# Kernel optimization log

Measured on AMD Instinct MI355X. Metric: run time of the kernel, lower is better.

## Reference

```python
import jax, jax.numpy as jnp
import numpy as np

N_HEAD = 16


def setup_inputs() -> dict:
    key = jax.random.key(0)
    k1, k2, k3 = jax.random.split(key, 3)
    B, T, C = 2, 2048, 1024
    x = jax.random.normal(k1, (B, T, C), dtype=jnp.float32)
    w_attn = jax.random.normal(k2, (C, 3 * C), dtype=jnp.float32) * 0.02
    w_proj = jax.random.normal(k3, (C, C), dtype=jnp.float32) * 0.02
    return {"x": x, "w_attn": w_attn, "w_proj": w_proj}


def reference(x, w_attn, w_proj):
    B, T, C = x.shape
    H = N_HEAD
    D = C // H
    qkv = x @ w_attn  # [B, T, 3C]
    q, k, v = jnp.split(qkv, 3, axis=2)
    q = q.reshape(B, T, H, D)
    k = k.reshape(B, T, H, D)
    v = v.reshape(B, T, H, D)
    scale = 1.0 / jnp.sqrt(jnp.asarray(D, dtype=x.dtype))
    # Full T x T score matrix, matching the 'standard_attention' path.
    att = jnp.einsum('bthd,bshd->bhts', q, k) * scale  # [B, H, T, T]
    causal = jnp.tril(jnp.ones((T, T), dtype=bool))
    att = jnp.where(causal[None, None, :, :], att, jnp.asarray(-jnp.inf, dtype=att.dtype))
    att = jax.nn.softmax(att, axis=-1)
    # dropout_p is False (== 0.0) in the original module, so no dropout applied.
    y = jnp.einsum('bhts,bshd->bthd', att, v)  # [B, T, H, D]
    y = y.reshape(B, T, C)
    return y @ w_proj
```

## Files before the change

### kernel.cpp

```cpp
#include <hip/hip_runtime.h>
#include <math.h>

#define BB 2
#define TT 2048
#define HH 16
#define DD 64
#define CC 1024
#define C3 3072

typedef __attribute__((ext_vector_type(8))) short bf16x8;
typedef __attribute__((ext_vector_type(4))) short bf16x4;
typedef __attribute__((ext_vector_type(4))) float f32x4;
typedef __attribute__((ext_vector_type(2))) unsigned int u32x2;

__device__ __forceinline__ unsigned short f2bf(float f) {
  union { float f; unsigned u; } v; v.f = f;
  unsigned r = v.u + 0x7fffu + ((v.u >> 16) & 1u);
  return (unsigned short)(r >> 16);
}
__device__ __forceinline__ unsigned short f2bf_up(float f) {
  union { float f; unsigned u; } v; v.f = f;
  return (unsigned short)((v.u + 0x8000u) >> 16);
}

__device__ __forceinline__ void async_cp16(const void* g, void* l) {
  __builtin_amdgcn_global_load_lds(
      (const __attribute__((address_space(1))) void*)g,
      (__attribute__((address_space(3))) void*)l, 16, 0, 0);
}

__global__ __launch_bounds__(256)
void prep(const float* __restrict__ x, const float* __restrict__ w_attn,
          const float* __restrict__ w_proj, unsigned short* __restrict__ xb,
          unsigned short* __restrict__ wat, unsigned short* __restrict__ wpt) {
  __shared__ __align__(16) float Ts[64][68];
  const int bx = blockIdx.x, tid = threadIdx.x;
  if (bx < 1024) {
    int i = bx * 256 + tid;
#pragma unroll
    for (int it = 0; it < 4; ++it, i += 262144) {
      const float4 v = ((const float4*)x)[i];
      bf16x4 o = {(short)f2bf(v.x), (short)f2bf(v.y),
                  (short)f2bf(v.z), (short)f2bf(v.w)};
      ((bf16x4*)xb)[i] = o;
    }
    return;
  }
  const float* W;
  unsigned short* WT;
  int Nd, bound, n0, k0;
  float s;
  if (bx < 1792) {
    const int bid = bx - 1024;
    W = w_attn; WT = wat; Nd = 3072; bound = 1024; s = 0.18033688f;
    n0 = (bid % 48) * 64; k0 = (bid / 48) * 64;
  } else {
    const int bid = bx - 1792;
    W = w_proj; WT = wpt; Nd = 1024; bound = 0; s = 1.0f;
    n0 = (bid % 16) * 64; k0 = (bid / 16) * 64;
  }
  const int rl = tid >> 4, c4 = tid & 15;
#pragma unroll
  for (int it = 0; it < 4; ++it) {
    const int r = it * 16 + rl;
    *(float4*)&Ts[r][c4 * 4] =
        *(const float4*)(W + (size_t)(k0 + r) * Nd + n0 + c4 * 4);
  }
  __syncthreads();
#pragma unroll
  for (int it = 0; it < 4; ++it) {
    const int n = it * 16 + rl;
    const float sc = (n0 + n < bound) ? s : 1.0f;
    bf16x4 o = {(short)f2bf(Ts[c4 * 4 + 0][n] * sc),
                (short)f2bf(Ts[c4 * 4 + 1][n] * sc),
                (short)f2bf(Ts[c4 * 4 + 2][n] * sc),
                (short)f2bf(Ts[c4 * 4 + 3][n] * sc)};
    *(bf16x4*)(WT + (size_t)(n0 + n) * CC + k0 + c4 * 4) = o;
  }
}

template <int MODE, int BM>
__global__ __launch_bounds__(256)
void gemm_bf16(const unsigned short* __restrict__ A,
               const unsigned short* __restrict__ BT,
               void* __restrict__ Cout, unsigned short* __restrict__ Vout,
               int M, int N, int K) {
  constexpr int MT = BM / 32;
  constexpr int ABYTES = BM * 64;
  __shared__ __align__(16) unsigned short As[2 * BM * 32];
  __shared__ __align__(16) unsigned short Bs[2 * 128 * 32];

  const int tid = threadIdx.x;
  const int w = tid >> 6, lane = tid & 63;
  const int l15 = lane & 15, quad = lane >> 4;
  const int wm = w >> 1, wn = w & 1;

  const int row0 = blockIdx.y * BM, col0 = blockIdx.x * 128;

  const int c0 = tid, c1 = tid + 256;
  const int ar0 = c0 >> 2, ak0 = ((c0 & 3) ^ ((c0 >> 3) & 3)) * 8;
  const int ar1 = c1 >> 2, ak1 = ((c1 & 3) ^ ((c1 >> 3) & 3)) * 8;
  const unsigned short* gA0 = A + (size_t)(row0 + ar0) * K + ak0;
  const unsigned short* gA1 = A + (size_t)(row0 + ar1) * K + ak1;
  const unsigned short* gB0 = BT + (size_t)(col0 + ar0) * K + ak0;
  const unsigned short* gB1 = BT + (size_t)(col0 + ar1) * K + ak1;
  const int lds0 = w * 1024, lds1 = 4096 + w * 1024;

  const int fro = l15 * 64 + 16 * (quad ^ ((l15 >> 1) & 3));

  f32x4 acc[MT][4];
#pragma unroll
  for (int i = 0; i < MT; ++i)
#pragma unroll
    for (int j = 0; j < 4; ++j) acc[i][j] = (f32x4){0.f, 0.f, 0.f, 0.f};

  const int nt = K / 32;
  async_cp16(gA0, (char*)As + lds0);
  if (BM == 128) async_cp16(gA1, (char*)As + lds1);
  async_cp16(gB0, (char*)Bs + lds0);
  async_cp16(gB1, (char*)Bs + lds1);

  for (int i = 0; i < nt; ++i) {
    const int cur = i & 1;
    __syncthreads();

    if (i + 1 < nt) {
      const int k1 = (i + 1) * 32;
      const int alt = cur ^ 1;
      async_cp16(gA0 + k1, (char*)As + alt * ABYTES + lds0);
      if (BM == 128) async_cp16(gA1 + k1, (char*)As + alt * ABYTES + lds1);
      async_cp16(gB0 + k1, (char*)Bs + alt * 8192 + lds0);
      async_cp16(gB1 + k1, (char*)Bs + alt * 8192 + lds1);
    }

    const char* fA = (const char*)As + cur * ABYTES + wm * (BM * 32) + fro;
    const char* fB = (const char*)Bs + cur * 8192 + wn * 4096 + fro;

    bf16x8 af[MT], bf[4];
#pragma unroll
    for (int mt = 0; mt < MT; ++mt) af[mt] = *(const bf16x8*)(fA + mt * 1024);
#pragma unroll
    for (int nt2 = 0; nt2 < 4; ++nt2) bf[nt2] = *(const bf16x8*)(fB + nt2 * 1024);
#pragma unroll
    for (int mt = 0; mt < MT; ++mt)
#pragma unroll
      for (int nt2 = 0; nt2 < 4; ++nt2)
        acc[mt][nt2] = __builtin_amdgcn_mfma_f32_16x16x32_bf16(
            af[mt], bf[nt2], acc[mt][nt2], 0, 0, 0);
  }

  if (MODE == 2 && col0 >= 2048) {
#pragma unroll
    for (int mt = 0; mt < MT; ++mt) {
      const int rbase = row0 + wm * (BM / 2) + mt * 16 + quad * 4;
      const int bq = rbase >> 11, t0 = rbase & 2047;
#pragma unroll
      for (int nt2 = 0; nt2 < 4; ++nt2) {
        const int col = col0 + wn * 64 + nt2 * 16 + l15;
        bf16x4 o = {(short)f2bf(acc[mt][nt2][0]), (short)f2bf(acc[mt][nt2][1]),
                    (short)f2bf(acc[mt][nt2][2]), (short)f2bf(acc[mt][nt2][3])};
        *(bf16x4*)(Vout + ((size_t)((bq << 10) + col - 2048) << 11) + t0) = o;
      }
    }
  } else if (MODE >= 1) {
    unsigned short* Cb = (unsigned short*)Cout;
#pragma unroll
    for (int mt = 0; mt < MT; ++mt) {
      const int rbase = row0 + wm * (BM / 2) + mt * 16 + quad * 4;
#pragma unroll
      for (int r = 0; r < 4; ++r) {
        unsigned short* cr = Cb + (size_t)(rbase + r) * N + col0 + wn * 64 + l15;
#pragma unroll
        for (int nt2 = 0; nt2 < 4; ++nt2) cr[nt2 * 16] = f2bf(acc[mt][nt2][r]);
      }
    }
  } else {
    float* Cf = (float*)Cout;
#pragma unroll
    for (int mt = 0; mt < MT; ++mt) {
      const int rbase = row0 + wm * (BM / 2) + mt * 16 + quad * 4;
#pragma unroll
      for (int r = 0; r < 4; ++r) {
        float* cr = Cf + (size_t)(rbase + r) * N + col0 + wn * 64 + l15;
#pragma unroll
        for (int nt2 = 0; nt2 < 4; ++nt2) cr[nt2 * 16] = acc[mt][nt2][r];
      }
    }
  }
}

__global__ __launch_bounds__(256)
void attn_mfma(const unsigned short* __restrict__ qkvb,
               const unsigned short* __restrict__ vt,
               unsigned short* __restrict__ y) {
  const int n = blockIdx.x;
  const int bh = (n & 7) + 8 * ((n >> 3) & 3);
  const int qpair = n >> 5;
  const int b = bh >> 4, h = bh & 15;
  const int tid = threadIdx.x;
  const int w = tid >> 6;
  const int lane = tid & 63;
  const int l15 = lane & 15, quad = lane >> 4;

  __shared__ __align__(16) char Kb[2 * 8192];
  __shared__ __align__(16) char Vb[2 * 8192];
  __shared__ __align__(16) unsigned short Ps[4 * 16 * 72];
  unsigned short* psw = Ps + w * 16 * 72;

  const int lr = lane >> 3;
  const int lc = lane & 7;
  const int srcoff = ((lc ^ lr) << 4);
  const char* ksrc = (const char*)qkvb + ((size_t)(b * TT) * C3 + 1024 + h * 64) * 2;
  const char* vsrc = (const char*)vt + ((size_t)(b * HH + h) * DD * TT) * 2;

  const int fro = l15 * 128 + ((quad ^ (l15 & 7)) << 4);

  bf16x8 onesf;
#pragma unroll
  for (int jj = 0; jj < 8; ++jj) onesf[jj] = (short)0x3F80;

  for (int phase = 0; phase < 2; ++phase) {
    const int qt = phase == 0 ? 31 - qpair : qpair;

    if (phase) __syncthreads();

    const unsigned short* qrow =
        qkvb + (size_t)(b * TT + qt * 64 + w * 16 + l15) * C3 + h * DD;
    bf16x8 qf0 = *(const bf16x8*)(qrow + quad * 8);
    bf16x8 qf1 = *(const bf16x8*)(qrow + 32 + quad * 8);

    f32x4 O[4];
#pragma unroll
    for (int dt = 0; dt < 4; ++dt) O[dt] = (f32x4){0.f, 0.f, 0.f, 0.f};
    f32x4 lacc = (f32x4){0.f, 0.f, 0.f, 0.f};

#pragma unroll
    for (int i = 0; i < 2; ++i) {
      async_cp16(ksrc + (size_t)(w * 16 + i * 8 + lr) * (C3 * 2) + srcoff,
                 Kb + w * 2048 + i * 1024);
      async_cp16(vsrc + (size_t)(w * 16 + i * 8 + lr) * (TT * 2) + srcoff,
                 Vb + w * 2048 + i * 1024);
    }

    for (int j = 0; j <= qt; ++j) {
      const int cur = j & 1;
      __syncthreads();

      if (j < qt) {
        const int key1 = (j + 1) * 64;
        char* kd = Kb + (cur ^ 1) * 8192 + w * 2048;
        char* vd = Vb + (cur ^ 1) * 8192 + w * 2048;
#pragma unroll
        for (int i = 0; i < 2; ++i) {
          async_cp16(
              ksrc + (size_t)(key1 + w * 16 + i * 8 + lr) * (C3 * 2) + srcoff,
              kd + i * 1024);
          async_cp16(
              vsrc + (size_t)(w * 16 + i * 8 + lr) * (TT * 2) + key1 * 2 + srcoff,
              vd + i * 1024);
        }
      }

      const char* Kc = Kb + cur * 8192;
      const char* Vc = Vb + cur * 8192;

      f32x4 S[4];
#pragma unroll
      for (int ct = 0; ct < 4; ++ct) {
        bf16x8 k0 = *(const bf16x8*)(Kc + ct * 2048 + fro);
        bf16x8 k1 = *(const bf16x8*)(Kc + ct * 2048 + (fro ^ 64));
        f32x4 z = (f32x4){-12.f, -12.f, -12.f, -12.f};
        z = __builtin_amdgcn_mfma_f32_16x16x32_bf16(k0, qf0, z, 0, 0, 0);
        z = __builtin_amdgcn_mfma_f32_16x16x32_bf16(k1, qf1, z, 0, 0, 0);
        S[ct] = z;
      }

      if (j == qt) {
#pragma unroll
        for (int ct = 0; ct < 4; ++ct)
#pragma unroll
          for (int r = 0; r < 4; ++r)
            if (16 * ct + quad * 4 + r > w * 16 + l15) S[ct][r] = -INFINITY;
      }

#pragma unroll
      for (int ct = 0; ct < 4; ++ct) {
        const unsigned p0 = f2bf_up(exp2f(S[ct][0]));
        const unsigned p1 = f2bf_up(exp2f(S[ct][1]));
        const unsigned p2 = f2bf_up(exp2f(S[ct][2]));
        const unsigned p3 = f2bf_up(exp2f(S[ct][3]));
        u32x2 d;
        d[0] = p0 | (p1 << 16);
        d[1] = p2 | (p3 << 16);
        *(u32x2*)((char*)psw + l15 * 144 + ct * 32 + quad * 8) = d;
      }

      bf16x8 pf0 = *(const bf16x8*)((char*)psw + l15 * 144 + quad * 16);
      bf16x8 pf1 = *(const bf16x8*)((char*)psw + l15 * 144 + 64 + quad * 16);

      lacc = __builtin_amdgcn_mfma_f32_16x16x32_bf16(onesf, pf0, lacc, 0, 0, 0);
      lacc = __builtin_amdgcn_mfma_f32_16x16x32_bf16(onesf, pf1, lacc, 0, 0, 0);
#pragma unroll
      for (int dt = 0; dt < 4; ++dt) {
        bf16x8 v0 = *(const bf16x8*)(Vc + dt * 2048 + fro);
        bf16x8 v1 = *(const bf16x8*)(Vc + dt * 2048 + (fro ^ 64));
        O[dt] = __builtin_amdgcn_mfma_f32_16x16x32_bf16(v0, pf0, O[dt], 0, 0, 0);
        O[dt] = __builtin_amdgcn_mfma_f32_16x16x32_bf16(v1, pf1, O[dt], 0, 0, 0);
      }
    }

    const float inv = 1.0f / lacc[0];
    unsigned short* yr =
        y + (size_t)(b * TT + qt * 64 + w * 16 + l15) * CC + h * DD + quad * 4;
#pragma unroll
    for (int dt = 0; dt < 4; ++dt) {
      bf16x4 o = {(short)f2bf(O[dt][0] * inv), (short)f2bf(O[dt][1] * inv),
                  (short)f2bf(O[dt][2] * inv), (short)f2bf(O[dt][3] * inv)};
      *(bf16x4*)(yr + dt * 16) = o;
    }
  }
}

extern "C" void kernel_launch(void* const* d_in, const int* in_sizes, int n_in,
                              void* d_out, int out_size, void* d_ws,
                              size_t ws_size, hipStream_t stream) {
  const float* x      = (const float*)d_in[0];
  const float* w_attn = (const float*)d_in[1];
  const float* w_proj = (const float*)d_in[2];
  float* out = (float*)d_out;

  unsigned short* xb   = (unsigned short*)d_ws;
  unsigned short* wat  = xb + (size_t)4096 * 1024;
  unsigned short* wpt  = wat + (size_t)3072 * 1024;
  unsigned short* qkvb = wpt + (size_t)1024 * 1024;
  unsigned short* vt   = qkvb + (size_t)4096 * 3072;
  unsigned short* yb   = vt + (size_t)BB * HH * DD * TT;

  dim3 blk(256);

  prep<<<2048, blk, 0, stream>>>(x, w_attn, w_proj, xb, wat, wpt);

  gemm_bf16<2, 128><<<dim3(C3 / 128, (BB * TT) / 128), blk, 0, stream>>>(
      xb, wat, qkvb, vt, BB * TT, C3, CC);

  attn_mfma<<<dim3(512, 1, 1), blk, 0, stream>>>(qkvb, vt, yb);

  gemm_bf16<0, 64><<<dim3(CC / 128, (BB * TT) / 64), blk, 0, stream>>>(
      yb, wpt, out, nullptr, BB * TT, CC, CC);
}
```

Before: 192.0 us.

## Specialize QKV and output GEMMs with retuned tiles and deeper K-steps

Replaces the templated GEMM with two dedicated kernels. The QKV GEMM now uses 128x192 tiles, giving 16x32=512 blocks (previously 24x32=768), with each wave covering all 128 rows and 48 columns. The output projection GEMM uses a K-step of 64 with a wider XOR swizzle, halving the number of barrier and loop iterations. Both kernels request two blocks per CU through launch bounds, and the larger accumulator arrays may raise register pressure.

```diff
diff --git a/kernel.cpp b/kernel.cpp
--- a/kernel.cpp
+++ b/kernel.cpp
@@ -79,112 +79,185 @@
   }
 }
 
-template <int MODE, int BM>
-__global__ __launch_bounds__(256)
-void gemm_bf16(const unsigned short* __restrict__ A,
-               const unsigned short* __restrict__ BT,
-               void* __restrict__ Cout, unsigned short* __restrict__ Vout,
-               int M, int N, int K) {
-  constexpr int MT = BM / 32;
-  constexpr int ABYTES = BM * 64;
-  __shared__ __align__(16) unsigned short As[2 * BM * 32];
-  __shared__ __align__(16) unsigned short Bs[2 * 128 * 32];
+__global__ __launch_bounds__(256, 2)
+void gemm_qkv(const unsigned short* __restrict__ A,
+              const unsigned short* __restrict__ BT,
+              unsigned short* __restrict__ Cb,
+              unsigned short* __restrict__ Vout) {
+  __shared__ __align__(16) unsigned short As[2 * 128 * 32];
+  __shared__ __align__(16) unsigned short Bs[2 * 192 * 32];
+
+  const int tid = threadIdx.x;
+  const int w = tid >> 6, lane = tid & 63;
+  const int l15 = lane & 15, quad = lane >> 4;
+  const int row0 = blockIdx.y * 128, col0 = blockIdx.x * 192;
+
+  const int ca0 = tid, ca1 = tid + 256;
+  const int ra0 = ca0 >> 2, ka0 = ((ca0 & 3) ^ ((ca0 >> 3) & 3)) * 8;
+  const int ra1 = ca1 >> 2, ka1 = ((ca1 & 3) ^ ((ca1 >> 3) & 3)) * 8;
+  const unsigned short* gA0 = A + (size_t)(row0 + ra0) * CC + ka0;
+  const unsigned short* gA1 = A + (size_t)(row0 + ra1) * CC + ka1;
+  const int cb0 = tid, cb1 = tid + 256, cb2 = tid + 512;
+  const int rb0 = cb0 >> 2, kb0 = ((cb0 & 3) ^ ((cb0 >> 3) & 3)) * 8;
+  const int rb1 = cb1 >> 2, kb1 = ((cb1 & 3) ^ ((cb1 >> 3) & 3)) * 8;
+  const int rb2 = cb2 >> 2, kb2 = ((cb2 & 3) ^ ((cb2 >> 3) & 3)) * 8;
+  const unsigned short* gB0 = BT + (size_t)(col0 + rb0) * CC + kb0;
+  const unsigned short* gB1 = BT + (size_t)(col0 + rb1) * CC + kb1;
+  const unsigned short* gB2 = BT + (size_t)(col0 + rb2) * CC + kb2;
+  const int la0 = tid * 16, la1 = tid * 16 + 4096;
+  const int lb0 = tid * 16, lb1 = tid * 16 + 4096, lb2 = tid * 16 + 8192;
+
+  const int fro = l15 * 64 + 16 * (quad ^ ((l15 >> 1) & 3));
+
+  f32x4 acc[8][3];
+#pragma unroll
+  for (int i = 0; i < 8; ++i)
+#pragma unroll
+    for (int j = 0; j < 3; ++j) acc[i][j] = (f32x4){0.f, 0.f, 0.f, 0.f};
+
+  async_cp16(gA0, (char*)As + la0);
+  async_cp16(gA1, (char*)As + la1);
+  async_cp16(gB0, (char*)Bs + lb0);
+  async_cp16(gB1, (char*)Bs + lb1);
+  async_cp16(gB2, (char*)Bs + lb2);
+
+  for (int i = 0; i < 32; ++i) {
+    const int cur = i & 1;
+    __syncthreads();
+
+    if (i + 1 < 32) {
+      const int k1 = (i + 1) * 32;
+      const int ab = (cur ^ 1) * 8192, bb = (cur ^ 1) * 12288;
+      async_cp16(gA0 + k1, (char*)As + ab + la0);
+      async_cp16(gA1 + k1, (char*)As + ab + la1);
+      async_cp16(gB0 + k1, (char*)Bs + bb + lb0);
+      async_cp16(gB1 + k1, (char*)Bs + bb + lb1);
+      async_cp16(gB2 + k1, (char*)Bs + bb + lb2);
+    }
+
+    const char* fA = (const char*)As + cur * 8192 + fro;
+    const char* fB = (const char*)Bs + cur * 12288 + w * 3072 + fro;
+
+    bf16x8 af[8], bf[3];
+#pragma unroll
+    for (int mt = 0; mt < 8; ++mt) af[mt] = *(const bf16x8*)(fA + mt * 1024);
+#pragma unroll
+    for (int nt = 0; nt < 3; ++nt) bf[nt] = *(const bf16x8*)(fB + nt * 1024);
+#pragma unroll
+    for (int mt = 0; mt < 8; ++mt)
+#pragma unroll
+      for (int nt = 0; nt < 3; ++nt)
+        acc[mt][nt] = __builtin_amdgcn_mfma_f32_16x16x32_bf16(
+            af[mt], bf[nt], acc[mt][nt], 0, 0, 0);
+  }
+
+#pragma unroll
+  for (int mt = 0; mt < 8; ++mt) {
+    const int rbase = row0 + mt * 16 + quad * 4;
+#pragma unroll
+    for (int nt = 0; nt < 3; ++nt) {
+      const int colb = col0 + w * 48 + nt * 16;
+      if (colb >= 2048) {
+        const int bq = rbase >> 11, t0 = rbase & 2047;
+        const int d = colb + l15 - 2048;
+        bf16x4 o = {(short)f2bf(acc[mt][nt][0]), (short)f2bf(acc[mt][nt][1]),
+                    (short)f2bf(acc[mt][nt][2]), (short)f2bf(acc[mt][nt][3])};
+        *(bf16x4*)(Vout + (((size_t)(bq << 10) + d) << 11) + t0) = o;
+      } else {
+        const int col = colb + l15;
+#pragma unroll
+        for (int r = 0; r < 4; ++r)
+          Cb[(size_t)(rbase + r) * C3 + col] = f2bf(acc[mt][nt][r]);
+      }
+    }
+  }
+}
+
+__global__ __launch_bounds__(256, 2)
+void gemm_out(const unsigned short* __restrict__ A,
+              const unsigned short* __restrict__ BT,
+              float* __restrict__ Cf) {
+  __shared__ __align__(16) unsigned short As[2 * 64 * 64];
+  __shared__ __align__(16) unsigned short Bs[2 * 128 * 64];
 
   const int tid = threadIdx.x;
   const int w = tid >> 6, lane = tid & 63;
   const int l15 = lane & 15, quad = lane >> 4;
   const int wm = w >> 1, wn = w & 1;
-
-  const int row0 = blockIdx.y * BM, col0 = blockIdx.x * 128;
-
-  const int c0 = tid, c1 = tid + 256;
-  const int ar0 = c0 >> 2, ak0 = ((c0 & 3) ^ ((c0 >> 3) & 3)) * 8;
-  const int ar1 = c1 >> 2, ak1 = ((c1 & 3) ^ ((c1 >> 3) & 3)) * 8;
-  const unsigned short* gA0 = A + (size_t)(row0 + ar0) * K + ak0;
-  const unsigned short* gA1 = A + (size_t)(row0 + ar1) * K + ak1;
-  const unsigned short* gB0 = BT + (size_t)(col0 + ar0) * K + ak0;
-  const unsigned short* gB1 = BT + (size_t)(col0 + ar1) * K + ak1;
-  const int lds0 = w * 1024, lds1 = 4096 + w * 1024;
-
-  const int fro = l15 * 64 + 16 * (quad ^ ((l15 >> 1) & 3));
-
-  f32x4 acc[MT][4];
-#pragma unroll
-  for (int i = 0; i < MT; ++i)
+  const int row0 = blockIdx.y * 64, col0 = blockIdx.x * 128;
+
+  const int ca0 = tid, ca1 = tid + 256;
+  const int ra0 = ca0 >> 3, ka0 = ((ca0 & 7) ^ ((ca0 >> 3) & 7)) * 8;
+  const int ra1 = ca1 >> 3, ka1 = ((ca1 & 7) ^ ((ca1 >> 3) & 7)) * 8;
+  const unsigned short* gA0 = A + (size_t)(row0 + ra0) * CC + ka0;
+  const unsigned short* gA1 = A + (size_t)(row0 + ra1) * CC + ka1;
+  const unsigned short* gB[4];
+  int lb[4];
+#pragma unroll
+  for (int t = 0; t < 4; ++t) {
+    const int c = tid + t * 256;
+    const int rb = c >> 3, kb = ((c & 7) ^ ((c >> 3) & 7)) * 8;
+    gB[t] = BT + (size_t)(col0 + rb) * CC + kb;
+    lb[t] = c * 16;
+  }
+  const int la0 = tid * 16, la1 = tid * 16 + 4096;
+
+  const int fro = l15 * 128 + ((quad ^ (l15 & 7)) << 4);
+
+  f32x4 acc[2][4];
+#pragma unroll
+  for (int i = 0; i < 2; ++i)
 #pragma unroll
     for (int j = 0; j < 4; ++j) acc[i][j] = (f32x4){0.f, 0.f, 0.f, 0.f};
 
-  const int nt = K / 32;
-  async_cp16(gA0, (char*)As + lds0);
-  if (BM == 128) async_cp16(gA1, (char*)As + lds1);
-  async_cp16(gB0, (char*)Bs + lds0);
-  async_cp16(gB1, (char*)Bs + lds1);
-
-  for (int i = 0; i < nt; ++i) {
+  async_cp16(gA0, (char*)As + la0);
+  async_cp16(gA1, (char*)As + la1);
+#pragma unroll
+  for (int t = 0; t < 4; ++t) async_cp16(gB[t], (char*)Bs + lb[t]);
+
+  for (int i = 0; i < 16; ++i) {
     const int cur = i & 1;
     __syncthreads();
 
-    if (i + 1 < nt) {
-      const int k1 = (i + 1) * 32;
-      const int alt = cur ^ 1;
-      async_cp16(gA0 + k1, (char*)As + alt * ABYTES + lds0);
-      if (BM == 128) async_cp16(gA1 + k1, (char*)As + alt * ABYTES + lds1);
-      async_cp16(gB0 + k1, (char*)Bs + alt * 8192 + lds0);
-      async_cp16(gB1 + k1, (char*)Bs + alt * 8192 + lds1);
-    }
-
-    const char* fA = (const char*)As + cur * ABYTES + wm * (BM * 32) + fro;
-    const char* fB = (const char*)Bs + cur * 8192 + wn * 4096 + fro;
-
-    bf16x8 af[MT], bf[4];
-#pragma unroll
-    for (int mt = 0; mt < MT; ++mt) af[mt] = *(const bf16x8*)(fA + mt * 1024);
-#pragma unroll
-    for (int nt2 = 0; nt2 < 4; ++nt2) bf[nt2] = *(const bf16x8*)(fB + nt2 * 1024);
-#pragma unroll
-    for (int mt = 0; mt < MT; ++mt)
-#pragma unroll
-      for (int nt2 = 0; nt2 < 4; ++nt2)
-        acc[mt][nt2] = __builtin_amdgcn_mfma_f32_16x16x32_bf16(
-            af[mt], bf[nt2], acc[mt][nt2], 0, 0, 0);
-  }
-
-  if (MODE == 2 && col0 >= 2048) {
-#pragma unroll
-    for (int mt = 0; mt < MT; ++mt) {
-      const int rbase = row0 + wm * (BM / 2) + mt * 16 + quad * 4;
-      const int bq = rbase >> 11, t0 = rbase & 2047;
-#pragma unroll
-      for (int nt2 = 0; nt2 < 4; ++nt2) {
-        const int col = col0 + wn * 64 + nt2 * 16 + l15;
-        bf16x4 o = {(short)f2bf(acc[mt][nt2][0]), (short)f2bf(acc[mt][nt2][1]),
-                    (short)f2bf(acc[mt][nt2][2]), (short)f2bf(acc[mt][nt2][3])};
-        *(bf16x4*)(Vout + ((size_t)((bq << 10) + col - 2048) << 11) + t0) = o;
-      }
-    }
-  } else if (MODE >= 1) {
-    unsigned short* Cb = (unsigned short*)Cout;
-#pragma unroll
-    for (int mt = 0; mt < MT; ++mt) {
-      const int rbase = row0 + wm * (BM / 2) + mt * 16 + quad * 4;
-#pragma unroll
-      for (int r = 0; r < 4; ++r) {
-        unsigned short* cr = Cb + (size_t)(rbase + r) * N + col0 + wn * 64 + l15;
-#pragma unroll
-        for (int nt2 = 0; nt2 < 4; ++nt2) cr[nt2 * 16] = f2bf(acc[mt][nt2][r]);
-      }
-    }
-  } else {
-    float* Cf = (float*)Cout;
-#pragma unroll
-    for (int mt = 0; mt < MT; ++mt) {
-      const int rbase = row0 + wm * (BM / 2) + mt * 16 + quad * 4;
-#pragma unroll
-      for (int r = 0; r < 4; ++r) {
-        float* cr = Cf + (size_t)(rbase + r) * N + col0 + wn * 64 + l15;
-#pragma unroll
-        for (int nt2 = 0; nt2 < 4; ++nt2) cr[nt2 * 16] = acc[mt][nt2][r];
-      }
+    if (i + 1 < 16) {
+      const int k1 = (i + 1) * 64;
+      const int ab = (cur ^ 1) * 8192, bb = (cur ^ 1) * 16384;
+      async_cp16(gA0 + k1, (char*)As + ab + la0);
+      async_cp16(gA1 + k1, (char*)As + ab + la1);
+#pragma unroll
+      for (int t = 0; t < 4; ++t) async_cp16(gB[t] + k1, (char*)Bs + bb + lb[t]);
+    }
+
+    const char* fA = (const char*)As + cur * 8192 + wm * 4096 + fro;
+    const char* fB = (const char*)Bs + cur * 16384 + wn * 8192 + fro;
+
+#pragma unroll
+    for (int kh = 0; kh < 2; ++kh) {
+      const int xo = kh * 64;
+      bf16x8 af[2], bf[4];
+#pragma unroll
+      for (int mt = 0; mt < 2; ++mt)
+        af[mt] = *(const bf16x8*)(fA + mt * 2048 + ((fro + xo) & 127) - (fro & 127));
+#pragma unroll
+      for (int nt = 0; nt < 4; ++nt)
+        bf[nt] = *(const bf16x8*)(fB + nt * 2048 + ((fro + xo) & 127) - (fro & 127));
+#pragma unroll
+      for (int mt = 0; mt < 2; ++mt)
+#pragma unroll
+        for (int nt = 0; nt < 4; ++nt)
+          acc[mt][nt] = __builtin_amdgcn_mfma_f32_16x16x32_bf16(
+              af[mt], bf[nt], acc[mt][nt], 0, 0, 0);
+    }
+  }
+
+#pragma unroll
+  for (int mt = 0; mt < 2; ++mt) {
+    const int rbase = row0 + wm * 32 + mt * 16 + quad * 4;
+#pragma unroll
+    for (int r = 0; r < 4; ++r) {
+      float* cr = Cf + (size_t)(rbase + r) * CC + col0 + wn * 64 + l15;
+#pragma unroll
+      for (int nt = 0; nt < 4; ++nt) cr[nt * 16] = acc[mt][nt][r];
     }
   }
 }
@@ -340,11 +413,10 @@
 
   prep<<<2048, blk, 0, stream>>>(x, w_attn, w_proj, xb, wat, wpt);
 
-  gemm_bf16<2, 128><<<dim3(C3 / 128, (BB * TT) / 128), blk, 0, stream>>>(
-      xb, wat, qkvb, vt, BB * TT, C3, CC);
+  gemm_qkv<<<dim3(C3 / 192, (BB * TT) / 128), blk, 0, stream>>>(
+      xb, wat, qkvb, vt);
 
   attn_mfma<<<dim3(512, 1, 1), blk, 0, stream>>>(qkvb, vt, yb);
 
-  gemm_bf16<0, 64><<<dim3(CC / 128, (BB * TT) / 64), blk, 0, stream>>>(
-      yb, wpt, out, nullptr, BB * TT, CC, CC);
-}
+  gemm_out<<<dim3(CC / 128, (BB * TT) / 64), blk, 0, stream>>>(yb, wpt, out);
+}
```

Result: faster. 184.1 us (-4.1%).
